# Performance work log

Hardware: AMD Instinct MI355X
Metric: run time of the kernel (lower is better)

## Reference

```python
import jax, jax.numpy as jnp
import numpy as np

HIDDEN = 2048
NUM_HEADS = 32
NUM_KV_HEADS = 8
HEAD_DIM = 64
ROPE_THETA = 10000.0


def _rope_tables(S, dtype=jnp.float32):
    freqs = 1.0 / (ROPE_THETA ** (jnp.arange(0, HEAD_DIM, 2, dtype=jnp.float32) / HEAD_DIM))
    angles = jnp.arange(S, dtype=jnp.float32)[:, None] * freqs[None, :]  # [S, D/2]
    return jnp.cos(angles).astype(dtype), jnp.sin(angles).astype(dtype)


def _apply_rope(x, cos, sin):
    # x: [B, H, S, D] with interleaved even/odd rotation pairs
    xe = x[..., 0::2]
    xo = x[..., 1::2]
    oe = xe * cos - xo * sin
    oo = xe * sin + xo * cos
    return jnp.stack([oe, oo], axis=-1).reshape(x.shape)


def setup_inputs() -> dict:
    key = jax.random.key(0)
    ks = jax.random.split(key, 5)
    scale = 0.02
    return {
        "x": jax.random.normal(ks[0], (2, 2048, HIDDEN), dtype=jnp.float32),
        "wq": jax.random.normal(ks[1], (NUM_HEADS * HEAD_DIM, HIDDEN), dtype=jnp.float32) * scale,
        "wk": jax.random.normal(ks[2], (NUM_KV_HEADS * HEAD_DIM, HIDDEN), dtype=jnp.float32) * scale,
        "wv": jax.random.normal(ks[3], (NUM_KV_HEADS * HEAD_DIM, HIDDEN), dtype=jnp.float32) * scale,
        "wo": jax.random.normal(ks[4], (HIDDEN, NUM_HEADS * HEAD_DIM), dtype=jnp.float32) * scale,
    }


def reference(x, wq, wk, wv, wo):
    B, S, _ = x.shape
    G = NUM_HEADS // NUM_KV_HEADS  # GQA group size

    q = (x @ wq.T).reshape(B, S, NUM_HEADS, HEAD_DIM).transpose(0, 2, 1, 3)      # [B,Hq,S,D]
    k = (x @ wk.T).reshape(B, S, NUM_KV_HEADS, HEAD_DIM).transpose(0, 2, 1, 3)   # [B,Hkv,S,D]
    v = (x @ wv.T).reshape(B, S, NUM_KV_HEADS, HEAD_DIM).transpose(0, 2, 1, 3)

    cos, sin = _rope_tables(S, x.dtype)
    q = _apply_rope(q, cos, sin)
    k = _apply_rope(k, cos, sin)

    # GQA without materializing repeated K/V: fold group dim into q
    qg = q.reshape(B, NUM_KV_HEADS, G, S, HEAD_DIM)
    scale = 1.0 / jnp.sqrt(jnp.asarray(HEAD_DIM, dtype=x.dtype))
    scores = jnp.einsum("bkgsd,bktd->bkgst", qg, k) * scale  # [B,Hkv,G,S,S]

    causal = jnp.tril(jnp.ones((S, S), dtype=bool))
    scores = jnp.where(causal, scores, jnp.finfo(scores.dtype).min)
    probs = jax.nn.softmax(scores, axis=-1)

    out = jnp.einsum("bkgst,bktd->bkgsd", probs, v)                 # [B,Hkv,G,S,D]
    out = out.reshape(B, NUM_HEADS, S, HEAD_DIM).transpose(0, 2, 1, 3).reshape(B, S, NUM_HEADS * HEAD_DIM)
    return out @ wo.T
```

## Files before the change

### kernel.cpp

```cpp
#include <hip/hip_runtime.h>
#include <hip/hip_bf16.h>

typedef __hip_bfloat16 bf16;
typedef __attribute__((ext_vector_type(8))) short short8;
typedef __attribute__((ext_vector_type(4))) float f32x4;

#define S_LEN 2048
#define BATCH 2
#define M_TOT 4096
#define HID 2048
#define NH 32
#define NKV 8
#define HD 64
#define KVD 512
#define QSCALE 0.125f

#define MFMA16(a, b, c) __builtin_amdgcn_mfma_f32_16x16x32_bf16(a, b, c, 0, 0, 0)

__device__ __forceinline__ void gload_lds16(const bf16* g, bf16* l) {
    __builtin_amdgcn_global_load_lds((const __attribute__((address_space(1))) void*)g,
                                     (__attribute__((address_space(3))) void*)l,
                                     16, 0, 0);
}

__device__ __forceinline__ float b2f(short v) {
    unsigned u = ((unsigned)(unsigned short)v) << 16;
    float f; __builtin_memcpy(&f, &u, 4); return f;
}

#define N8_X   1048576
#define N8_WQ   524288
#define N8_WK   131072
#define N8_TOT 2359296
__global__ void cast_all_kernel(const float* __restrict__ x, const float* __restrict__ wq,
                                const float* __restrict__ wk, const float* __restrict__ wv,
                                const float* __restrict__ wo, bf16* __restrict__ dst) {
    int stride = gridDim.x * blockDim.x;
    for (int i = blockIdx.x * blockDim.x + threadIdx.x; i < N8_TOT; i += stride) {
        const float* s; int off;
        if (i < N8_X)                        { s = x;  off = i; }
        else if (i < N8_X + N8_WQ)           { s = wq; off = i - N8_X; }
        else if (i < N8_X + N8_WQ + N8_WK)   { s = wk; off = i - (N8_X + N8_WQ); }
        else if (i < N8_X + N8_WQ + 2*N8_WK) { s = wv; off = i - (N8_X + N8_WQ + N8_WK); }
        else                                 { s = wo; off = i - (N8_X + N8_WQ + 2*N8_WK); }
        const float4* sp = (const float4*)(s + (size_t)off * 8);
        float4 a = sp[0], b = sp[1];
        bf16 tmp[8];
        tmp[0] = __float2bfloat16(a.x); tmp[1] = __float2bfloat16(a.y);
        tmp[2] = __float2bfloat16(a.z); tmp[3] = __float2bfloat16(a.w);
        tmp[4] = __float2bfloat16(b.x); tmp[5] = __float2bfloat16(b.y);
        tmp[6] = __float2bfloat16(b.z); tmp[7] = __float2bfloat16(b.w);
        *(short8*)(dst + (size_t)i * 8) = *(short8*)tmp;
    }
}

__global__ void rope_tables_kernel(float* __restrict__ cosb, float* __restrict__ sinb) {
    int idx = blockIdx.x * blockDim.x + threadIdx.x;
    if (idx >= S_LEN * 32) return;
    int s = idx >> 5, d = idx & 31;
    float freq = powf(10000.0f, -(float)(2 * d) / 64.0f);
    float ang = (float)s * freq;
    cosb[idx] = cosf(ang);
    sinb[idx] = sinf(ang);
}

__device__ __forceinline__ short8 rope8(short8 v, float4 c, float4 s, float scale) {
    short8 o;
    const float* cp = (const float*)&c;
    const float* sp = (const float*)&s;
    #pragma unroll
    for (int m = 0; m < 4; m++) {
        float xe = b2f(v[2 * m]) * scale;
        float xo = b2f(v[2 * m + 1]) * scale;
        bf16 oe = __float2bfloat16(xe * cp[m] - xo * sp[m]);
        bf16 oo = __float2bfloat16(xe * sp[m] + xo * cp[m]);
        short se, so;
        __builtin_memcpy(&se, &oe, 2); __builtin_memcpy(&so, &oo, 2);
        o[2 * m] = se; o[2 * m + 1] = so;
    }
    return o;
}

__device__ __forceinline__ void gemm_core(const bf16* __restrict__ A,
                                          const bf16* __restrict__ W,
                                          int K, int m0, int n0,
                                          bf16* As, bf16* Bs,
                                          f32x4 acc[4][4]) {
    int tid = threadIdx.x;
    int lane = tid & 63, wid = tid >> 6;
    int wr = wid >> 1, wc = wid & 1;
    int lhi = lane >> 4, llo = lane & 15;
    int c0 = tid, c1 = tid + 256;
    int r0 = c0 >> 2, s0 = ((c0 & 3) ^ ((r0 >> 1) & 3)) * 8;
    int r1 = c1 >> 2, s1 = ((c1 & 3) ^ ((r1 >> 1) & 3)) * 8;
    const bf16* gA0 = A + (size_t)(m0 + r0) * K + s0;
    const bf16* gA1 = A + (size_t)(m0 + r1) * K + s1;
    const bf16* gB0 = W + (size_t)(n0 + r0) * K + s0;
    const bf16* gB1 = W + (size_t)(n0 + r1) * K + s1;

    auto stage = [&](int buf, int k0) {
        bf16* a = As + buf * 4096;
        bf16* b = Bs + buf * 4096;
        gload_lds16(gA0 + k0, a + c0 * 8);
        gload_lds16(gA1 + k0, a + c1 * 8);
        gload_lds16(gB0 + k0, b + c0 * 8);
        gload_lds16(gB1 + k0, b + c1 * 8);
    };
    auto compute = [&](int buf) {
        const bf16* Ac = As + buf * 4096;
        const bf16* Bc = Bs + buf * 4096;
        short8 af[4], bfr[4];
        #pragma unroll
        for (int i = 0; i < 4; i++) {
            int row = wr * 64 + i * 16 + llo;
            af[i] = *(const short8*)(Ac + row * 32 + ((lhi ^ ((row >> 1) & 3)) * 8));
        }
        #pragma unroll
        for (int j = 0; j < 4; j++) {
            int row = wc * 64 + j * 16 + llo;
            bfr[j] = *(const short8*)(Bc + row * 32 + ((lhi ^ ((row >> 1) & 3)) * 8));
        }
        __builtin_amdgcn_s_setprio(1);
        #pragma unroll
        for (int i = 0; i < 4; i++)
            #pragma unroll
            for (int j = 0; j < 4; j++)
                acc[i][j] = MFMA16(af[i], bfr[j], acc[i][j]);
        __builtin_amdgcn_s_setprio(0);
    };

    int nt = K / 32;
    stage(0, 0);
    stage(1, 32);
    int b0 = 0, b1 = 1, b2 = 2;
    for (int t = 0; t < nt - 1; ++t) {
        asm volatile("s_waitcnt vmcnt(4)" ::: "memory");
        __builtin_amdgcn_s_barrier();
        if (t + 2 < nt) stage(b2, (t + 2) * 32);
        __builtin_amdgcn_sched_barrier(0);
        compute(b0);
        int tmp = b0; b0 = b1; b1 = b2; b2 = tmp;
    }
    asm volatile("s_waitcnt vmcnt(0)" ::: "memory");
    __builtin_amdgcn_s_barrier();
    compute(b0);
}

__global__ __launch_bounds__(256) void gemm_qkv_kernel(
        const bf16* __restrict__ xb,
        const bf16* __restrict__ wq, const bf16* __restrict__ wk, const bf16* __restrict__ wv,
        const float* __restrict__ cosb, const float* __restrict__ sinb,
        bf16* __restrict__ qb, bf16* __restrict__ kb, bf16* __restrict__ vtb) {
    __shared__ bf16 As[3 * 128 * 32];
    __shared__ bf16 Bs[3 * 128 * 32];
    int by = blockIdx.y;
    const bf16* W; bf16* Cb; int n0, ldc, mode;
    if (by < 16)      { W = wq; Cb = qb;  n0 = by * 128;        ldc = 2048; mode = 0; }
    else if (by < 20) { W = wk; Cb = kb;  n0 = (by - 16) * 128; ldc = 512;  mode = 2; }
    else              { W = wv; Cb = vtb; n0 = (by - 20) * 128; ldc = 0;    mode = 1; }
    int bx = blockIdx.x;
    int bxs = (bx & 7) * 4 + (bx >> 3);
    int m0 = bxs * 128;

    f32x4 acc[4][4] = {};
    gemm_core(xb, W, HID, m0, n0, As, Bs, acc);

    int lane = threadIdx.x & 63, wid = threadIdx.x >> 6;
    int wr = wid >> 1, wc = wid & 1;
    int lhi = lane >> 4, llo = lane & 15;
    #pragma unroll
    for (int i = 0; i < 4; i++)
        #pragma unroll
        for (int j = 0; j < 4; j++) {
            int col = wc * 64 + j * 16 + llo;
            #pragma unroll
            for (int r = 0; r < 4; r++) {
                int row = wr * 64 + i * 16 + lhi * 4 + r;
                int m = m0 + row;
                float v = acc[i][j][r];
                if (mode == 0) {
                    Cb[(size_t)m * ldc + n0 + col] = __float2bfloat16(v);
                } else if (mode == 1) {
                    int bb = m >> 11, ss = m & 2047;
                    Cb[((size_t)(bb * 512 + n0 + col)) * S_LEN + ss] = __float2bfloat16(v);
                } else {
                    int dcol = n0 + col;
                    int dd = dcol & 63;
                    int pidx = dd >> 1;
                    float sgn = (dd & 1) ? 1.0f : -1.0f;
                    int ss = m & 2047;
                    float c  = cosb[ss * 32 + pidx];
                    float sn = sinb[ss * 32 + pidx];
                    float o = __shfl_xor(v, 1, 64);
                    float outv = v * c + sgn * o * sn;
                    Cb[(size_t)m * 512 + dcol] = __float2bfloat16(outv);
                }
            }
        }
}

__global__ __launch_bounds__(256) void gemm_out_kernel(
        const bf16* __restrict__ attnb, const bf16* __restrict__ wob,
        float* __restrict__ out) {
    __shared__ bf16 As[3 * 128 * 32];
    __shared__ bf16 Bs[3 * 128 * 32];
    int bx = blockIdx.x;
    int bxs = (bx & 7) * 4 + (bx >> 3);
    int m0 = bxs * 128;
    int n0 = blockIdx.y * 128;
    f32x4 acc[4][4] = {};
    gemm_core(attnb, wob, HID, m0, n0, As, Bs, acc);

    int lane = threadIdx.x & 63, wid = threadIdx.x >> 6;
    int wr = wid >> 1, wc = wid & 1;
    int lhi = lane >> 4, llo = lane & 15;
    #pragma unroll
    for (int i = 0; i < 4; i++)
        #pragma unroll
        for (int j = 0; j < 4; j++) {
            int col = wc * 64 + j * 16 + llo;
            #pragma unroll
            for (int r = 0; r < 4; r++) {
                int row = wr * 64 + i * 16 + lhi * 4 + r;
                out[(size_t)(m0 + row) * HID + n0 + col] = acc[i][j][r];
            }
        }
}

__global__ __launch_bounds__(256, 4) void flash_kernel(
        const bf16* __restrict__ qb, const bf16* __restrict__ kb,
        const bf16* __restrict__ vtb, const float* __restrict__ cosb,
        const float* __restrict__ sinb, bf16* __restrict__ attnb) {
    __shared__ bf16 Ks[2][64 * 64];
    __shared__ bf16 Vs[2][64 * 64];
    __shared__ bf16 Pl[4][16 * 64];
    int bh = blockIdx.y;
    int b = bh >> 5, h = bh & 31;
    int kvh = h >> 2;
    int tid = threadIdx.x;
    int wid = tid >> 6, lane = tid & 63;
    int lhi = lane >> 4, llo = lane & 15;

    const bf16* Kg = kb + (size_t)(b * S_LEN) * KVD + kvh * HD;
    const bf16* Vg = vtb + (size_t)(b * 512 + kvh * 64) * S_LEN;

    int c0 = tid, c1 = tid + 256;
    int r0 = c0 >> 3, s0 = ((c0 & 7) ^ (r0 & 7)) * 8;
    int r1 = c1 >> 3, s1 = ((c1 & 7) ^ (r1 & 7)) * 8;

    bf16* pl = &Pl[wid][0];
    const int xw = llo & 7;
    const int hh = lhi >> 1;
    bf16* pwb = pl + llo * 64 + (lhi & 1) * 4;
    const int prd0 = llo * 64 + ((lhi ^ xw) * 8);
    const int prd1 = llo * 64 + (((lhi + 4) ^ xw) * 8);

    auto stage = [&](int buf, int t0) {
        gload_lds16(Kg + (size_t)(t0 + r0) * KVD + s0, &Ks[buf][c0 * 8]);
        gload_lds16(Kg + (size_t)(t0 + r1) * KVD + s1, &Ks[buf][c1 * 8]);
        gload_lds16(Vg + (size_t)r0 * S_LEN + t0 + s0, &Vs[buf][c0 * 8]);
        gload_lds16(Vg + (size_t)r1 * S_LEN + t0 + s1, &Vs[buf][c1 * 8]);
    };

    auto run_phase = [&](int j) {
        int qrow0 = j * 64 + wid * 16;
        int spos = qrow0 + llo;
        const bf16* qrow = qb + ((size_t)(b * S_LEN) + spos) * (NH * HD) + h * HD;
        float4 cv0 = *(const float4*)(cosb + spos * 32 + lhi * 4);
        float4 sv0 = *(const float4*)(sinb + spos * 32 + lhi * 4);
        float4 cv1 = *(const float4*)(cosb + spos * 32 + 16 + lhi * 4);
        float4 sv1 = *(const float4*)(sinb + spos * 32 + 16 + lhi * 4);
        short8 qf0 = rope8(*(const short8*)(qrow + lhi * 8), cv0, sv0, QSCALE);
        short8 qf1 = rope8(*(const short8*)(qrow + 32 + lhi * 8), cv1, sv1, QSCALE);

        f32x4 acc[4] = {};
        float psum = 0.f;
        int qloc = wid * 16 + llo;

        stage(0, 0);
        asm volatile("s_waitcnt vmcnt(0)" ::: "memory");
        __builtin_amdgcn_s_barrier();
        int cur = 0;
        for (int t = 0; t <= j; ++t) {
            int t0 = t * 64;
            if (t < j) stage(cur ^ 1, t0 + 64);
            const bf16* Kc = &Ks[cur][0];
            const bf16* Vc = &Vs[cur][0];
            f32x4 z[4];
            __builtin_amdgcn_s_setprio(1);
            #pragma unroll
            for (int cb = 0; cb < 4; cb++) {
                int row = cb * 16 + llo;
                short8 k0 = *(const short8*)(Kc + row * 64 + ((lhi ^ xw) * 8));
                short8 k1 = *(const short8*)(Kc + row * 64 + (((lhi + 4) ^ xw) * 8));
                f32x4 zz = {0.f, 0.f, 0.f, 0.f};
                zz = MFMA16(k0, qf0, zz);
                zz = MFMA16(k1, qf1, zz);
                z[cb] = zz;
            }
            __builtin_amdgcn_s_setprio(0);
            bool diag = (t == j);
            #pragma unroll
            for (int cb = 0; cb < 4; cb++) {
                float p0 = __expf(z[cb][0]);
                float p1 = __expf(z[cb][1]);
                float p2 = __expf(z[cb][2]);
                float p3 = __expf(z[cb][3]);
                if (diag) {
                    int kl = cb * 16 + lhi * 4;
                    p0 = (kl + 0 <= qloc) ? p0 : 0.f;
                    p1 = (kl + 1 <= qloc) ? p1 : 0.f;
                    p2 = (kl + 2 <= qloc) ? p2 : 0.f;
                    p3 = (kl + 3 <= qloc) ? p3 : 0.f;
                }
                psum += (p0 + p1) + (p2 + p3);
                bf16 tmp[4];
                tmp[0] = __float2bfloat16(p0); tmp[1] = __float2bfloat16(p1);
                tmp[2] = __float2bfloat16(p2); tmp[3] = __float2bfloat16(p3);
                *(uint2*)(pwb + (((2 * cb + hh) ^ xw) * 8)) = *(uint2*)tmp;
            }
            short8 pa0 = *(const short8*)(pl + prd0);
            short8 pa1 = *(const short8*)(pl + prd1);
            __builtin_amdgcn_s_setprio(1);
            #pragma unroll
            for (int jb = 0; jb < 4; jb++) {
                int row = jb * 16 + llo;
                short8 v0 = *(const short8*)(Vc + row * 64 + ((lhi ^ xw) * 8));
                short8 v1 = *(const short8*)(Vc + row * 64 + (((lhi + 4) ^ xw) * 8));
                acc[jb] = MFMA16(pa0, v0, acc[jb]);
                acc[jb] = MFMA16(pa1, v1, acc[jb]);
            }
            __builtin_amdgcn_s_setprio(0);
            asm volatile("s_waitcnt vmcnt(0)" ::: "memory");
            __builtin_amdgcn_s_barrier();
            cur ^= 1;
        }
        psum += __shfl_xor(psum, 16, 64);
        psum += __shfl_xor(psum, 32, 64);
        float inv[4];
        #pragma unroll
        for (int r = 0; r < 4; r++)
            inv[r] = 1.0f / __shfl(psum, lhi * 4 + r, 64);
        size_t obase = ((size_t)(b * S_LEN) + qrow0) * (NH * HD) + h * HD;
        #pragma unroll
        for (int jb = 0; jb < 4; jb++)
            #pragma unroll
            for (int r = 0; r < 4; r++)
                attnb[obase + (size_t)(lhi * 4 + r) * (NH * HD) + jb * 16 + llo] =
                    __float2bfloat16(acc[jb][r] * inv[r]);
    };

    run_phase(blockIdx.x);
    run_phase(31 - blockIdx.x);
}

extern "C" void kernel_launch(void* const* d_in, const int* in_sizes, int n_in,
                              void* d_out, int out_size, void* d_ws, size_t ws_size,
                              hipStream_t stream) {
    const float* x  = (const float*)d_in[0];
    const float* wq = (const float*)d_in[1];
    const float* wk = (const float*)d_in[2];
    const float* wv = (const float*)d_in[3];
    const float* wo = (const float*)d_in[4];
    float* out = (float*)d_out;

    char* ws = (char*)d_ws;
    size_t off = 0;
    auto alloc = [&](size_t bytes) { void* p = ws + off; off += (bytes + 255) & ~(size_t)255; return p; };
    bf16* xb   = (bf16*)alloc((size_t)M_TOT * HID * 2);
    bf16* wqb  = (bf16*)alloc((size_t)HID * HID * 2);
    bf16* wkb  = (bf16*)alloc((size_t)512 * HID * 2);
    bf16* wvb  = (bf16*)alloc((size_t)512 * HID * 2);
    bf16* wob  = (bf16*)alloc((size_t)HID * HID * 2);
    bf16* qb   = (bf16*)alloc((size_t)M_TOT * 2048 * 2);
    bf16* kb   = (bf16*)alloc((size_t)M_TOT * 512 * 2);
    bf16* vtb  = (bf16*)alloc((size_t)M_TOT * 512 * 2);
    bf16* attnb= (bf16*)alloc((size_t)M_TOT * 2048 * 2);
    float* cosb= (float*)alloc((size_t)S_LEN * 32 * 4);
    float* sinb= (float*)alloc((size_t)S_LEN * 32 * 4);

    cast_all_kernel<<<2048, 256, 0, stream>>>(x, wq, wk, wv, wo, xb);

    rope_tables_kernel<<<(S_LEN * 32 + 255) / 256, 256, 0, stream>>>(cosb, sinb);

    gemm_qkv_kernel<<<dim3(M_TOT / 128, 24), 256, 0, stream>>>(xb, wqb, wkb, wvb,
                                                               cosb, sinb, qb, kb, vtb);

    flash_kernel<<<dim3(16, BATCH * NH), 256, 0, stream>>>(qb, kb, vtb, cosb, sinb, attnb);

    gemm_out_kernel<<<dim3(M_TOT / 128, HID / 128), 256, 0, stream>>>(attnb, wob, out);
}
```

Measured before the change: 192.9 us.

## Fuse paired causal query tiles into one KV sweep sharing K/V loads

Instead of running two sequential phases per block (query tile j and 31-j), each with its own pass over K/V, the kernel now runs a single KV loop up to the longer tile. Each staged K/V tile and its V fragments are reused by both query tiles, with the shorter tile's work predicated off once it passes its diagonal. This roughly halves global-to-LDS K/V traffic and barriers for the short tile. It costs more registers (two accumulators and two Q fragments), which may pressure occupancy under launch_bounds(256,4).

```diff
diff --git a/kernel.cpp b/kernel.cpp
--- a/kernel.cpp
+++ b/kernel.cpp
@@ -240,6 +240,7 @@
     int tid = threadIdx.x;
     int wid = tid >> 6, lane = tid & 63;
     int lhi = lane >> 4, llo = lane & 15;
+    int jA = blockIdx.x, jB = 31 - jA;
 
     const bf16* Kg = kb + (size_t)(b * S_LEN) * KVD + kvh * HD;
     const bf16* Vg = vtb + (size_t)(b * 512 + kvh * 64) * S_LEN;
@@ -262,50 +263,78 @@
         gload_lds16(Vg + (size_t)r1 * S_LEN + t0 + s1, &Vs[buf][c1 * 8]);
     };
 
-    auto run_phase = [&](int j) {
-        int qrow0 = j * 64 + wid * 16;
-        int spos = qrow0 + llo;
-        const bf16* qrow = qb + ((size_t)(b * S_LEN) + spos) * (NH * HD) + h * HD;
-        float4 cv0 = *(const float4*)(cosb + spos * 32 + lhi * 4);
-        float4 sv0 = *(const float4*)(sinb + spos * 32 + lhi * 4);
-        float4 cv1 = *(const float4*)(cosb + spos * 32 + 16 + lhi * 4);
-        float4 sv1 = *(const float4*)(sinb + spos * 32 + 16 + lhi * 4);
-        short8 qf0 = rope8(*(const short8*)(qrow + lhi * 8), cv0, sv0, QSCALE);
-        short8 qf1 = rope8(*(const short8*)(qrow + 32 + lhi * 8), cv1, sv1, QSCALE);
-
-        f32x4 acc[4] = {};
-        float psum = 0.f;
-        int qloc = wid * 16 + llo;
-
-        stage(0, 0);
-        asm volatile("s_waitcnt vmcnt(0)" ::: "memory");
-        __builtin_amdgcn_s_barrier();
-        int cur = 0;
-        for (int t = 0; t <= j; ++t) {
-            int t0 = t * 64;
-            if (t < j) stage(cur ^ 1, t0 + 64);
-            const bf16* Kc = &Ks[cur][0];
-            const bf16* Vc = &Vs[cur][0];
-            f32x4 z[4];
-            __builtin_amdgcn_s_setprio(1);
+    int qrowA0 = jA * 64 + wid * 16;
+    int qrowB0 = jB * 64 + wid * 16;
+    short8 qfA0, qfA1, qfB0, qfB1;
+    {
+        int sposA = qrowA0 + llo;
+        const bf16* qr = qb + ((size_t)(b * S_LEN) + sposA) * (NH * HD) + h * HD;
+        float4 c0v = *(const float4*)(cosb + sposA * 32 + lhi * 4);
+        float4 s0v = *(const float4*)(sinb + sposA * 32 + lhi * 4);
+        float4 c1v = *(const float4*)(cosb + sposA * 32 + 16 + lhi * 4);
+        float4 s1v = *(const float4*)(sinb + sposA * 32 + 16 + lhi * 4);
+        qfA0 = rope8(*(const short8*)(qr + lhi * 8), c0v, s0v, QSCALE);
+        qfA1 = rope8(*(const short8*)(qr + 32 + lhi * 8), c1v, s1v, QSCALE);
+    }
+    {
+        int sposB = qrowB0 + llo;
+        const bf16* qr = qb + ((size_t)(b * S_LEN) + sposB) * (NH * HD) + h * HD;
+        float4 c0v = *(const float4*)(cosb + sposB * 32 + lhi * 4);
+        float4 s0v = *(const float4*)(sinb + sposB * 32 + lhi * 4);
+        float4 c1v = *(const float4*)(cosb + sposB * 32 + 16 + lhi * 4);
+        float4 s1v = *(const float4*)(sinb + sposB * 32 + 16 + lhi * 4);
+        qfB0 = rope8(*(const short8*)(qr + lhi * 8), c0v, s0v, QSCALE);
+        qfB1 = rope8(*(const short8*)(qr + 32 + lhi * 8), c1v, s1v, QSCALE);
+    }
+
+    f32x4 accA[4] = {}, accB[4] = {};
+    float psumA = 0.f, psumB = 0.f;
+    int qloc = wid * 16 + llo;
+
+    stage(0, 0);
+    asm volatile("s_waitcnt vmcnt(0)" ::: "memory");
+    __builtin_amdgcn_s_barrier();
+    int cur = 0;
+    for (int t = 0; t <= jB; ++t) {
+        int t0 = t * 64;
+        if (t < jB) stage(cur ^ 1, t0 + 64);
+        const bf16* Kc = &Ks[cur][0];
+        const bf16* Vc = &Vs[cur][0];
+        bool doA = (t <= jA);
+        f32x4 zA[4], zB[4];
+        __builtin_amdgcn_s_setprio(1);
+        #pragma unroll
+        for (int cb = 0; cb < 4; cb++) {
+            int row = cb * 16 + llo;
+            short8 k0 = *(const short8*)(Kc + row * 64 + ((lhi ^ xw) * 8));
+            short8 k1 = *(const short8*)(Kc + row * 64 + (((lhi + 4) ^ xw) * 8));
+            f32x4 zz = {0.f, 0.f, 0.f, 0.f};
+            zz = MFMA16(k0, qfB0, zz);
+            zz = MFMA16(k1, qfB1, zz);
+            zB[cb] = zz;
+            if (doA) {
+                f32x4 yy = {0.f, 0.f, 0.f, 0.f};
+                yy = MFMA16(k0, qfA0, yy);
+                yy = MFMA16(k1, qfA1, yy);
+                zA[cb] = yy;
+            }
+        }
+        __builtin_amdgcn_s_setprio(0);
+        short8 vf0[4], vf1[4];
+        #pragma unroll
+        for (int jb = 0; jb < 4; jb++) {
+            int row = jb * 16 + llo;
+            vf0[jb] = *(const short8*)(Vc + row * 64 + ((lhi ^ xw) * 8));
+            vf1[jb] = *(const short8*)(Vc + row * 64 + (((lhi + 4) ^ xw) * 8));
+        }
+        if (doA) {
+            bool diag = (t == jA);
             #pragma unroll
             for (int cb = 0; cb < 4; cb++) {
-                int row = cb * 16 + llo;
-                short8 k0 = *(const short8*)(Kc + row * 64 + ((lhi ^ xw) * 8));
-                short8 k1 = *(const short8*)(Kc + row * 64 + (((lhi + 4) ^ xw) * 8));
-                f32x4 zz = {0.f, 0.f, 0.f, 0.f};
-                zz = MFMA16(k0, qf0, zz);
-                zz = MFMA16(k1, qf1, zz);
-                z[cb] = zz;
-            }
-            __builtin_amdgcn_s_setprio(0);
-            bool diag = (t == j);
-            #pragma unroll
-            for (int cb = 0; cb < 4; cb++) {
-                float p0 = __expf(z[cb][0]);
-                float p1 = __expf(z[cb][1]);
-                float p2 = __expf(z[cb][2]);
-                float p3 = __expf(z[cb][3]);
+                float p0 = __expf(zA[cb][0]);
+                float p1 = __expf(zA[cb][1]);
+                float p2 = __expf(zA[cb][2]);
+                float p3 = __expf(zA[cb][3]);
                 if (diag) {
                     int kl = cb * 16 + lhi * 4;
                     p0 = (kl + 0 <= qloc) ? p0 : 0.f;
@@ -313,7 +342,7 @@
                     p2 = (kl + 2 <= qloc) ? p2 : 0.f;
                     p3 = (kl + 3 <= qloc) ? p3 : 0.f;
                 }
-                psum += (p0 + p1) + (p2 + p3);
+                psumA += (p0 + p1) + (p2 + p3);
                 bf16 tmp[4];
                 tmp[0] = __float2bfloat16(p0); tmp[1] = __float2bfloat16(p1);
                 tmp[2] = __float2bfloat16(p2); tmp[3] = __float2bfloat16(p3);
@@ -324,34 +353,68 @@
             __builtin_amdgcn_s_setprio(1);
             #pragma unroll
             for (int jb = 0; jb < 4; jb++) {
-                int row = jb * 16 + llo;
-                short8 v0 = *(const short8*)(Vc + row * 64 + ((lhi ^ xw) * 8));
-                short8 v1 = *(const short8*)(Vc + row * 64 + (((lhi + 4) ^ xw) * 8));
-                acc[jb] = MFMA16(pa0, v0, acc[jb]);
-                acc[jb] = MFMA16(pa1, v1, acc[jb]);
+                accA[jb] = MFMA16(pa0, vf0[jb], accA[jb]);
+                accA[jb] = MFMA16(pa1, vf1[jb], accA[jb]);
             }
             __builtin_amdgcn_s_setprio(0);
-            asm volatile("s_waitcnt vmcnt(0)" ::: "memory");
-            __builtin_amdgcn_s_barrier();
-            cur ^= 1;
-        }
-        psum += __shfl_xor(psum, 16, 64);
-        psum += __shfl_xor(psum, 32, 64);
-        float inv[4];
-        #pragma unroll
-        for (int r = 0; r < 4; r++)
-            inv[r] = 1.0f / __shfl(psum, lhi * 4 + r, 64);
-        size_t obase = ((size_t)(b * S_LEN) + qrow0) * (NH * HD) + h * HD;
-        #pragma unroll
-        for (int jb = 0; jb < 4; jb++)
-            #pragma unroll
-            for (int r = 0; r < 4; r++)
-                attnb[obase + (size_t)(lhi * 4 + r) * (NH * HD) + jb * 16 + llo] =
-                    __float2bfloat16(acc[jb][r] * inv[r]);
-    };
-
-    run_phase(blockIdx.x);
-    run_phase(31 - blockIdx.x);
+        }
+        {
+            bool diag = (t == jB);
+            #pragma unroll
+            for (int cb = 0; cb < 4; cb++) {
+                float p0 = __expf(zB[cb][0]);
+                float p1 = __expf(zB[cb][1]);
+                float p2 = __expf(zB[cb][2]);
+                float p3 = __expf(zB[cb][3]);
+                if (diag) {
+                    int kl = cb * 16 + lhi * 4;
+                    p0 = (kl + 0 <= qloc) ? p0 : 0.f;
+                    p1 = (kl + 1 <= qloc) ? p1 : 0.f;
+                    p2 = (kl + 2 <= qloc) ? p2 : 0.f;
+                    p3 = (kl + 3 <= qloc) ? p3 : 0.f;
+                }
+                psumB += (p0 + p1) + (p2 + p3);
+                bf16 tmp[4];
+                tmp[0] = __float2bfloat16(p0); tmp[1] = __float2bfloat16(p1);
+                tmp[2] = __float2bfloat16(p2); tmp[3] = __float2bfloat16(p3);
+                *(uint2*)(pwb + (((2 * cb + hh) ^ xw) * 8)) = *(uint2*)tmp;
+            }
+            short8 pb0 = *(const short8*)(pl + prd0);
+            short8 pb1 = *(const short8*)(pl + prd1);
+            __builtin_amdgcn_s_setprio(1);
+            #pragma unroll
+            for (int jb = 0; jb < 4; jb++) {
+                accB[jb] = MFMA16(pb0, vf0[jb], accB[jb]);
+                accB[jb] = MFMA16(pb1, vf1[jb], accB[jb]);
+            }
+            __builtin_amdgcn_s_setprio(0);
+        }
+        asm volatile("s_waitcnt vmcnt(0)" ::: "memory");
+        __builtin_amdgcn_s_barrier();
+        cur ^= 1;
+    }
+    psumA += __shfl_xor(psumA, 16, 64);
+    psumA += __shfl_xor(psumA, 32, 64);
+    psumB += __shfl_xor(psumB, 16, 64);
+    psumB += __shfl_xor(psumB, 32, 64);
+    float invA[4], invB[4];
+    #pragma unroll
+    for (int r = 0; r < 4; r++) {
+        invA[r] = 1.0f / __shfl(psumA, lhi * 4 + r, 64);
+        invB[r] = 1.0f / __shfl(psumB, lhi * 4 + r, 64);
+    }
+    size_t obaseA = ((size_t)(b * S_LEN) + qrowA0) * (NH * HD) + h * HD;
+    size_t obaseB = ((size_t)(b * S_LEN) + qrowB0) * (NH * HD) + h * HD;
+    #pragma unroll
+    for (int jb = 0; jb < 4; jb++)
+        #pragma unroll
+        for (int r = 0; r < 4; r++) {
+            int row = lhi * 4 + r;
+            attnb[obaseA + (size_t)row * (NH * HD) + jb * 16 + llo] =
+                __float2bfloat16(accA[jb][r] * invA[r]);
+            attnb[obaseB + (size_t)row * (NH * HD) + jb * 16 + llo] =
+                __float2bfloat16(accB[jb][r] * invB[r]);
+        }
 }
 
 extern "C" void kernel_launch(void* const* d_in, const int* in_sizes, int n_in,
```

Result: slower. 237.3 us (+23.0%).

## Replace QKV projection GEMM with 256x256-tile, 512-thread double-buffered kernel

Applied to the files above, without the earlier changes.

The QKV projection moves from a 128x128 tile, 256-thread kernel with a triple-buffered K=32 pipeline to a 256x256 tile kernel with 512 threads (8 waves) and K=64 steps. Each k-step is split into four quarter-phases that interleave global-to-LDS loads with MFMA work, and the LDS layout uses an XOR swizzle. Larger tiles raise arithmetic intensity and cut redundant loads of x and the weights. The grid shrinks to 192 blocks, which may underfill the 256 CUs, and the 128 KB of LDS per block limits occupancy to one block per CU.

```diff
diff --git a/kernel.cpp b/kernel.cpp
--- a/kernel.cpp
+++ b/kernel.cpp
@@ -81,6 +81,127 @@
     return o;
 }
 
+__global__ __launch_bounds__(512, 1) void gemm_qkv256_kernel(
+        const bf16* __restrict__ xb,
+        const bf16* __restrict__ wq, const bf16* __restrict__ wk, const bf16* __restrict__ wv,
+        const float* __restrict__ cosb, const float* __restrict__ sinb,
+        bf16* __restrict__ qb, bf16* __restrict__ kb, bf16* __restrict__ vtb) {
+    __shared__ bf16 As[2][256 * 64];
+    __shared__ bf16 Bs[2][256 * 64];
+    int tid = threadIdx.x;
+    int lane = tid & 63, w = tid >> 6;
+    int wr = w >> 2, wc = w & 3;
+    int lhi = lane >> 4, llo = lane & 15;
+
+    int by = blockIdx.y;
+    const bf16* W; int n0, mode;
+    if (by < 8)       { W = wq; n0 = by * 256;        mode = 0; }
+    else if (by < 10) { W = wk; n0 = (by - 8) * 256;  mode = 2; }
+    else              { W = wv; n0 = (by - 10) * 256; mode = 1; }
+    int bx = blockIdx.x;
+    int bxs = (bx & 7) * 2 + (bx >> 3);
+    int m0 = bxs * 256;
+
+    const bf16* Abase = xb + (size_t)m0 * HID;
+    const bf16* Bbase = W + (size_t)n0 * HID;
+
+    auto stage_half = [&](int buf, int kt, int h) {
+        const bf16* mat = (h < 2) ? Abase : Bbase;
+        bf16* ldsb = (h < 2) ? &As[buf][0] : &Bs[buf][0];
+        int h1 = h & 1;
+        #pragma unroll
+        for (int q2 = 0; q2 < 2; q2++) {
+            int gc = h1 * 1024 + q2 * 512 + tid;
+            int row = gc >> 3;
+            int sl = (gc & 7) ^ (row & 7);
+            gload_lds16(mat + (size_t)row * HID + kt * 64 + sl * 8, ldsb + gc * 8);
+        }
+    };
+
+    f32x4 acc[8][4] = {};
+    const int nt = HID / 64;
+
+    stage_half(0, 0, 0); stage_half(0, 0, 1);
+    stage_half(0, 0, 2); stage_half(0, 0, 3);
+    stage_half(1, 1, 2); stage_half(1, 1, 3);
+    asm volatile("s_waitcnt vmcnt(4)" ::: "memory");
+    __builtin_amdgcn_s_barrier();
+
+    for (int t = 0; t < nt; ++t) {
+        int bt = t & 1;
+        const bf16* Ac = &As[bt][0];
+        const bf16* Bc = &Bs[bt][0];
+        short8 bfr[4][2];
+        #pragma unroll
+        for (int q = 0; q < 4; q++) {
+            if (q == 0) {
+                #pragma unroll
+                for (int j = 0; j < 4; j++) {
+                    int row = wc * 64 + j * 16 + llo;
+                    int x = row & 7;
+                    bfr[j][0] = *(const short8*)(Bc + row * 64 + ((lhi ^ x) * 8));
+                    bfr[j][1] = *(const short8*)(Bc + row * 64 + (((4 + lhi) ^ x) * 8));
+                }
+            }
+            short8 a0[2], a1[2];
+            #pragma unroll
+            for (int i2 = 0; i2 < 2; i2++) {
+                int row = wr * 128 + (q * 2 + i2) * 16 + llo;
+                int x = row & 7;
+                a0[i2] = *(const short8*)(Ac + row * 64 + ((lhi ^ x) * 8));
+                a1[i2] = *(const short8*)(Ac + row * 64 + (((4 + lhi) ^ x) * 8));
+            }
+            if (q == 0) { if (t + 1 < nt) stage_half((t + 1) & 1, t + 1, 0); }
+            else if (q == 1) { if (t + 1 < nt) stage_half((t + 1) & 1, t + 1, 1); }
+            else if (q == 2) { if (t + 2 < nt) stage_half(bt, t + 2, 2); }
+            else             { if (t + 2 < nt) stage_half(bt, t + 2, 3); }
+            __builtin_amdgcn_s_barrier();
+            asm volatile("s_waitcnt lgkmcnt(0)" ::: "memory");
+            __builtin_amdgcn_sched_barrier(0);
+            __builtin_amdgcn_s_setprio(1);
+            #pragma unroll
+            for (int i2 = 0; i2 < 2; i2++)
+                #pragma unroll
+                for (int j = 0; j < 4; j++) {
+                    acc[q * 2 + i2][j] = MFMA16(a0[i2], bfr[j][0], acc[q * 2 + i2][j]);
+                    acc[q * 2 + i2][j] = MFMA16(a1[i2], bfr[j][1], acc[q * 2 + i2][j]);
+                }
+            __builtin_amdgcn_s_setprio(0);
+            if (q == 3)
+                asm volatile("s_waitcnt vmcnt(4)" ::: "memory");
+            __builtin_amdgcn_s_barrier();
+        }
+    }
+
+    #pragma unroll
+    for (int i = 0; i < 8; i++)
+        #pragma unroll
+        for (int j = 0; j < 4; j++) {
+            int col = wc * 64 + j * 16 + llo;
+            #pragma unroll
+            for (int r = 0; r < 4; r++) {
+                int m = m0 + wr * 128 + i * 16 + lhi * 4 + r;
+                float v = acc[i][j][r];
+                if (mode == 0) {
+                    qb[(size_t)m * 2048 + n0 + col] = __float2bfloat16(v);
+                } else if (mode == 1) {
+                    int bb = m >> 11, ss = m & 2047;
+                    vtb[((size_t)(bb * 512 + n0 + col)) * S_LEN + ss] = __float2bfloat16(v);
+                } else {
+                    int dcol = n0 + col;
+                    int dd = dcol & 63;
+                    int pidx = dd >> 1;
+                    float sgn = (dd & 1) ? 1.0f : -1.0f;
+                    int ss = m & 2047;
+                    float c  = cosb[ss * 32 + pidx];
+                    float sn = sinb[ss * 32 + pidx];
+                    float o = __shfl_xor(v, 1, 64);
+                    kb[(size_t)m * 512 + dcol] = __float2bfloat16(v * c + sgn * o * sn);
+                }
+            }
+        }
+}
+
 __device__ __forceinline__ void gemm_core(const bf16* __restrict__ A,
                                           const bf16* __restrict__ W,
                                           int K, int m0, int n0,
@@ -144,59 +265,6 @@
     asm volatile("s_waitcnt vmcnt(0)" ::: "memory");
     __builtin_amdgcn_s_barrier();
     compute(b0);
-}
-
-__global__ __launch_bounds__(256) void gemm_qkv_kernel(
-        const bf16* __restrict__ xb,
-        const bf16* __restrict__ wq, const bf16* __restrict__ wk, const bf16* __restrict__ wv,
-        const float* __restrict__ cosb, const float* __restrict__ sinb,
-        bf16* __restrict__ qb, bf16* __restrict__ kb, bf16* __restrict__ vtb) {
-    __shared__ bf16 As[3 * 128 * 32];
-    __shared__ bf16 Bs[3 * 128 * 32];
-    int by = blockIdx.y;
-    const bf16* W; bf16* Cb; int n0, ldc, mode;
-    if (by < 16)      { W = wq; Cb = qb;  n0 = by * 128;        ldc = 2048; mode = 0; }
-    else if (by < 20) { W = wk; Cb = kb;  n0 = (by - 16) * 128; ldc = 512;  mode = 2; }
-    else              { W = wv; Cb = vtb; n0 = (by - 20) * 128; ldc = 0;    mode = 1; }
-    int bx = blockIdx.x;
-    int bxs = (bx & 7) * 4 + (bx >> 3);
-    int m0 = bxs * 128;
-
-    f32x4 acc[4][4] = {};
-    gemm_core(xb, W, HID, m0, n0, As, Bs, acc);
-
-    int lane = threadIdx.x & 63, wid = threadIdx.x >> 6;
-    int wr = wid >> 1, wc = wid & 1;
-    int lhi = lane >> 4, llo = lane & 15;
-    #pragma unroll
-    for (int i = 0; i < 4; i++)
-        #pragma unroll
-        for (int j = 0; j < 4; j++) {
-            int col = wc * 64 + j * 16 + llo;
-            #pragma unroll
-            for (int r = 0; r < 4; r++) {
-                int row = wr * 64 + i * 16 + lhi * 4 + r;
-                int m = m0 + row;
-                float v = acc[i][j][r];
-                if (mode == 0) {
-                    Cb[(size_t)m * ldc + n0 + col] = __float2bfloat16(v);
-                } else if (mode == 1) {
-                    int bb = m >> 11, ss = m & 2047;
-                    Cb[((size_t)(bb * 512 + n0 + col)) * S_LEN + ss] = __float2bfloat16(v);
-                } else {
-                    int dcol = n0 + col;
-                    int dd = dcol & 63;
-                    int pidx = dd >> 1;
-                    float sgn = (dd & 1) ? 1.0f : -1.0f;
-                    int ss = m & 2047;
-                    float c  = cosb[ss * 32 + pidx];
-                    float sn = sinb[ss * 32 + pidx];
-                    float o = __shfl_xor(v, 1, 64);
-                    float outv = v * c + sgn * o * sn;
-                    Cb[(size_t)m * 512 + dcol] = __float2bfloat16(outv);
-                }
-            }
-        }
 }
 
 __global__ __launch_bounds__(256) void gemm_out_kernel(
@@ -383,8 +451,8 @@
 
     rope_tables_kernel<<<(S_LEN * 32 + 255) / 256, 256, 0, stream>>>(cosb, sinb);
 
-    gemm_qkv_kernel<<<dim3(M_TOT / 128, 24), 256, 0, stream>>>(xb, wqb, wkb, wvb,
-                                                               cosb, sinb, qb, kb, vtb);
+    gemm_qkv256_kernel<<<dim3(16, 12), 512, 0, stream>>>(xb, wqb, wkb, wvb,
+                                                         cosb, sinb, qb, kb, vtb);
 
     flash_kernel<<<dim3(16, BATCH * NH), 256, 0, stream>>>(qb, kb, vtb, cosb, sinb, attnb);
 
```

New measurement: 214.1 us. +11.0%, slower.
